# Kernel tuning notes

Measured on AMD Instinct MI355X. Metric: run time of the kernel, lower is better.

Reference implementation:

```python
import jax, jax.numpy as jnp
import numpy as np

D_MODEL = 1024
N_HEADS = 16
MAX_LEN = 2048
B, T = 2, 2048


def _rope_tables(seq_len, d_model):
    # NOTE: inv_freq spans full d_model (not d_head), matching the source module,
    # since RoPE is applied to q/k of shape (B, T, D) before the head split.
    inv_freq = 1.0 / 10000 ** (jnp.arange(0, d_model, 2, dtype=jnp.float32) / d_model)
    pos = jnp.arange(seq_len, dtype=jnp.float32)
    freqs = jnp.outer(pos, inv_freq)            # (T, D/2)
    return jnp.cos(freqs), jnp.sin(freqs)


def _apply_rope(x, cos, sin):
    # x: (B, T, D); cos/sin: (T, D/2)
    c = jnp.repeat(cos, 2, axis=-1)[None]       # (1, T, D)
    s = jnp.repeat(sin, 2, axis=-1)[None]
    xr = x.reshape(x.shape[0], x.shape[1], -1, 2)
    x_rot = jnp.stack([-xr[..., 1], xr[..., 0]], axis=-1).reshape(x.shape)
    return x * c + x_rot * s


def setup_inputs() -> dict:
    key = jax.random.key(0)
    ks = jax.random.split(key, 5)
    scale = 1.0 / np.sqrt(D_MODEL)
    x = jax.random.normal(ks[0], (B, T, D_MODEL), dtype=jnp.float32)
    wq = jax.random.normal(ks[1], (D_MODEL, D_MODEL), dtype=jnp.float32) * scale
    wk = jax.random.normal(ks[2], (D_MODEL, D_MODEL), dtype=jnp.float32) * scale
    wv = jax.random.normal(ks[3], (D_MODEL, D_MODEL), dtype=jnp.float32) * scale
    wo = jax.random.normal(ks[4], (D_MODEL, D_MODEL), dtype=jnp.float32) * scale
    mask = jnp.tril(jnp.ones((T, T), dtype=bool))[None, None]  # (1,1,T,T) causal
    return {"x": x, "mask": mask, "wq": wq, "wk": wk, "wv": wv, "wo": wo}


def reference(x, mask, wq, wk, wv, wo):
    Bn, Tn, Dn = x.shape
    d_head = Dn // N_HEADS
    cos, sin = _rope_tables(Tn, Dn)
    q = _apply_rope(x @ wq, cos, sin)
    k = _apply_rope(x @ wk, cos, sin)
    v = x @ wv
    q = q.reshape(Bn, Tn, N_HEADS, d_head).transpose(0, 2, 1, 3)  # (B,H,T,dh)
    k = k.reshape(Bn, Tn, N_HEADS, d_head).transpose(0, 2, 1, 3)
    v = v.reshape(Bn, Tn, N_HEADS, d_head).transpose(0, 2, 1, 3)
    scores = jnp.einsum('bhqd,bhkd->bhqk', q, k) / jnp.sqrt(jnp.float32(d_head))
    scores = jnp.where(mask, scores, jnp.float32(-1e10))
    attn = jax.nn.softmax(scores, axis=-1)
    out = jnp.einsum('bhqk,bhkd->bhqd', attn, v)
    out = out.transpose(0, 2, 1, 3).reshape(Bn, Tn, Dn)
    return out @ wo
```

## Files before the change

kernel.cpp:

```cpp
#include <hip/hip_runtime.h>
#include <hip/hip_bf16.h>

#define D_MODEL 1024
#define N_HEADS 16
#define DH      64
#define BATCH   2
#define SEQ     2048
#define M_ROWS  (BATCH*SEQ)

using f32x4  = __attribute__((ext_vector_type(4)))  float;
using f32x16 = __attribute__((ext_vector_type(16))) float;
using bfx8   = __attribute__((ext_vector_type(8)))  short;

__device__ __forceinline__ float bf2f(unsigned short u){
    unsigned int v = ((unsigned int)u) << 16;
    float f; __builtin_memcpy(&f, &v, 4); return f;
}
__device__ __forceinline__ unsigned short f2bf(float f){
    unsigned int u; __builtin_memcpy(&u, &f, 4);
    u = (u + 0x7FFFu + ((u >> 16) & 1u)) >> 16;
    return (unsigned short)u;
}
__device__ __forceinline__ unsigned int cvtpk_bf16(float lo, float hi){
    unsigned int r;
    asm("v_cvt_pk_bf16_f32 %0, %1, %2" : "=v"(r) : "v"(lo), "v"(hi));
    return r;
}

typedef __attribute__((address_space(3))) void as3_void;
typedef __attribute__((address_space(1))) const void as1_cvoid;
__device__ __forceinline__ void gload16(const void* g, void* l){
    __builtin_amdgcn_global_load_lds((as1_cvoid*)g, (as3_void*)l, 16, 0, 0);
}

__global__ void cast_x_kernel(const float* __restrict__ x, unsigned short* __restrict__ xb){
    int i = blockIdx.x*blockDim.x + threadIdx.x;
    float4 v = reinterpret_cast<const float4*>(x)[i];
    ushort4 o; o.x=f2bf(v.x); o.y=f2bf(v.y); o.z=f2bf(v.z); o.w=f2bf(v.w);
    reinterpret_cast<ushort4*>(xb)[i] = o;
}

__global__ void transpose_cast_w(const float* __restrict__ w0, const float* __restrict__ w1,
                                 const float* __restrict__ w2, const float* __restrict__ w3,
                                 unsigned short* __restrict__ o0, unsigned short* __restrict__ o1,
                                 unsigned short* __restrict__ o2, unsigned short* __restrict__ o3){
    __shared__ float tile[32][33];
    const float* w; unsigned short* o;
    switch (blockIdx.z){
        case 0:  w=w0; o=o0; break;
        case 1:  w=w1; o=o1; break;
        case 2:  w=w2; o=o2; break;
        default: w=w3; o=o3; break;
    }
    const int tx = threadIdx.x, ty = threadIdx.y;
    const int x0 = blockIdx.x*32, y0 = blockIdx.y*32;
    #pragma unroll
    for (int j=0;j<32;j+=8) tile[ty+j][tx] = w[(size_t)(y0+ty+j)*D_MODEL + x0 + tx];
    __syncthreads();
    #pragma unroll
    for (int j=0;j<32;j+=8) o[(size_t)(x0+ty+j)*D_MODEL + y0 + tx] = f2bf(tile[tx][ty+j]);
}

__global__ __launch_bounds__(256) void gemm_qkv(const unsigned short* __restrict__ A,
                                                const unsigned short* __restrict__ Bq,
                                                const unsigned short* __restrict__ Bk,
                                                const unsigned short* __restrict__ Bv,
                                                unsigned short* __restrict__ Qo,
                                                unsigned short* __restrict__ Ko,
                                                unsigned short* __restrict__ Vto){
    __shared__ unsigned short As[64*64];
    __shared__ unsigned short Bs[128*64];
    const int bid  = blockIdx.x;
    const int xcdg = bid & 7;
    const int i    = bid >> 3;
    const int yt   = xcdg*8 + (i & 7);
    const int xsel = i >> 3;
    const int sel  = xsel >> 3;
    const int n0   = (xsel & 7) * 128;
    const unsigned short* Bt = (sel==0) ? Bq : ((sel==1) ? Bk : Bv);
    const int tid = threadIdx.x;
    const int lane = tid & 63, wid = tid >> 6;
    const int l15 = lane & 15, hi = lane >> 4;
    const int wr = wid >> 1, wc = wid & 1;
    const int m0 = yt * 64;

    f32x4 acc[2][4] = {};

    for (int kt = 0; kt < D_MODEL; kt += 64){
        __syncthreads();
        #pragma unroll
        for (int i2 = 0; i2 < 2; ++i2){
            int c = tid + 256*i2;
            int row = c >> 3, ch = c & 7;
            int sc = ch ^ (row & 7);
            gload16(A + (size_t)(m0 + row)*D_MODEL + kt + sc*8, As + c*8);
        }
        #pragma unroll
        for (int i2 = 0; i2 < 4; ++i2){
            int c = tid + 256*i2;
            int row = c >> 3, ch = c & 7;
            int sc = ch ^ (row & 7);
            gload16(Bt + (size_t)(n0 + row)*D_MODEL + kt + sc*8, Bs + c*8);
        }
        asm volatile("s_waitcnt vmcnt(0)" ::: "memory");
        __syncthreads();
        #pragma unroll
        for (int ks = 0; ks < 2; ++ks){
            bfx8 a[2], b[4];
            #pragma unroll
            for (int t = 0; t < 2; ++t){
                const int ra = 32*wr + 16*t + l15;
                a[t] = *reinterpret_cast<const bfx8*>(As + ra*64 + (((ks*4 + hi) ^ (ra & 7))*8));
            }
            #pragma unroll
            for (int t = 0; t < 4; ++t){
                const int rb = 64*wc + 16*t + l15;
                b[t] = *reinterpret_cast<const bfx8*>(Bs + rb*64 + (((ks*4 + hi) ^ (rb & 7))*8));
            }
            #pragma unroll
            for (int rt = 0; rt < 2; ++rt)
                #pragma unroll
                for (int ct = 0; ct < 4; ++ct)
                    acc[rt][ct] = __builtin_amdgcn_mfma_f32_16x16x32_bf16(a[rt], b[ct], acc[rt][ct], 0, 0, 0);
        }
    }

    if (sel < 2){
        unsigned short* o = sel ? Ko : Qo;
        const float cfac = -0.02595256269f;
        float invf[4];
        #pragma unroll
        for (int ct = 0; ct < 4; ++ct){
            const int n = n0 + 64*wc + 16*ct + l15;
            invf[ct] = exp2f(cfac * (float)(n >> 1));
        }
        #pragma unroll
        for (int rt = 0; rt < 2; ++rt)
            #pragma unroll
            for (int ct = 0; ct < 4; ++ct){
                const int m = m0 + 32*wr + 16*rt + 4*hi;
                const int n = n0 + 64*wc + 16*ct + l15;
                #pragma unroll
                for (int r=0;r<4;++r){
                    float v = acc[rt][ct][r];
                    float prt = __shfl_xor(v, 1);
                    int tpos = (m + r) & (SEQ-1);
                    float ang = (float)tpos * invf[ct];
                    float sv = __sinf(ang), cv = __cosf(ang);
                    float rot = (n & 1) ? __builtin_fmaf(v, cv,  prt*sv)
                                        : __builtin_fmaf(v, cv, -(prt*sv));
                    o[(size_t)(m+r)*D_MODEL + n] = f2bf(rot);
                }
            }
    } else {
        #pragma unroll
        for (int rt = 0; rt < 2; ++rt)
            #pragma unroll
            for (int ct = 0; ct < 4; ++ct){
                const int m = m0 + 32*wr + 16*rt + 4*hi;
                const int n = n0 + 64*wc + 16*ct + l15;
                const int b  = m >> 11, t = m & (SEQ-1);
                const int h  = n >> 6,  d = n & 63;
                ushort4 pk;
                pk.x = f2bf(acc[rt][ct][0]); pk.y = f2bf(acc[rt][ct][1]);
                pk.z = f2bf(acc[rt][ct][2]); pk.w = f2bf(acc[rt][ct][3]);
                *reinterpret_cast<ushort4*>(Vto + ((size_t)((b*N_HEADS + h)*DH + d))*SEQ + t) = pk;
            }
    }
}

__global__ __launch_bounds__(256) void gemm_out(const unsigned short* __restrict__ A,
                                                const unsigned short* __restrict__ Bt,
                                                float* __restrict__ dst){
    __shared__ unsigned short As[64*64];
    __shared__ unsigned short Bs[128*64];
    const int tid = threadIdx.x;
    const int lane = tid & 63, wid = tid >> 6;
    const int l15 = lane & 15, hi = lane >> 4;
    const int wr = wid >> 1, wc = wid & 1;
    const int m0 = blockIdx.y * 64, n0 = blockIdx.x * 128;

    f32x4 acc[2][4] = {};

    for (int kt = 0; kt < D_MODEL; kt += 64){
        __syncthreads();
        #pragma unroll
        for (int i = 0; i < 2; ++i){
            int c = tid + 256*i;
            int row = c >> 3, ch = c & 7;
            int sc = ch ^ (row & 7);
            gload16(A + (size_t)(m0 + row)*D_MODEL + kt + sc*8, As + c*8);
        }
        #pragma unroll
        for (int i = 0; i < 4; ++i){
            int c = tid + 256*i;
            int row = c >> 3, ch = c & 7;
            int sc = ch ^ (row & 7);
            gload16(Bt + (size_t)(n0 + row)*D_MODEL + kt + sc*8, Bs + c*8);
        }
        asm volatile("s_waitcnt vmcnt(0)" ::: "memory");
        __syncthreads();
        #pragma unroll
        for (int ks = 0; ks < 2; ++ks){
            bfx8 a[2], b[4];
            #pragma unroll
            for (int t = 0; t < 2; ++t){
                const int ra = 32*wr + 16*t + l15;
                a[t] = *reinterpret_cast<const bfx8*>(As + ra*64 + (((ks*4 + hi) ^ (ra & 7))*8));
            }
            #pragma unroll
            for (int t = 0; t < 4; ++t){
                const int rb = 64*wc + 16*t + l15;
                b[t] = *reinterpret_cast<const bfx8*>(Bs + rb*64 + (((ks*4 + hi) ^ (rb & 7))*8));
            }
            #pragma unroll
            for (int rt = 0; rt < 2; ++rt)
                #pragma unroll
                for (int ct = 0; ct < 4; ++ct)
                    acc[rt][ct] = __builtin_amdgcn_mfma_f32_16x16x32_bf16(a[rt], b[ct], acc[rt][ct], 0, 0, 0);
        }
    }

    #pragma unroll
    for (int rt = 0; rt < 2; ++rt)
        #pragma unroll
        for (int ct = 0; ct < 4; ++ct){
            const int m = m0 + 32*wr + 16*rt + 4*hi;
            const int n = n0 + 64*wc + 16*ct + l15;
            #pragma unroll
            for (int r=0;r<4;++r) dst[(size_t)(m+r)*D_MODEL + n] = acc[rt][ct][r];
        }
}

__global__ __launch_bounds__(256, 2) void attn_kernel(const unsigned short* __restrict__ Q,
                                                      const unsigned short* __restrict__ K,
                                                      const unsigned short* __restrict__ Vt,
                                                      unsigned short* __restrict__ O){
    __shared__ float Olds[3][64][64];
    __shared__ float Llds[3][64];

    const int tid = threadIdx.x;
    const int lane = tid & 63, wid = tid >> 6;
    const int l31 = lane & 31, hi2 = (lane >> 5) & 1;
    const int bid = blockIdx.x;
    const int xcd = bid & 7, j = bid >> 3;
    const int hp  = xcd*4 + (j & 3);
    const int b = hp >> 4, h = hp & 15;
    const int qt2 = 31 - (j >> 2);
    const int skmax = 2*qt2 + 1;
    const int qrowA = qt2*64 + l31;
    const int qrowB = qrowA + 32;

    const unsigned short* Kbase = K  + (size_t)(b*SEQ)*D_MODEL + h*DH + 8*hi2;
    const unsigned short* Vbase = Vt + ((size_t)((b*N_HEADS + h)*DH))*SEQ + 8*hi2;
    const float k2 = 0.18033688011f;

    bfx8 qfA[4], qfB[4];
    {
        const unsigned short* qa = Q + ((size_t)(b*SEQ) + qrowA)*D_MODEL + h*DH + 8*hi2;
        const unsigned short* qb = Q + ((size_t)(b*SEQ) + qrowB)*D_MODEL + h*DH + 8*hi2;
        #pragma unroll
        for (int m=0;m<4;++m){
            qfA[m] = *reinterpret_cast<const bfx8*>(qa + 16*m);
            qfB[m] = *reinterpret_cast<const bfx8*>(qb + 16*m);
        }
    }

    f32x16 oaccA[2] = {}, oaccB[2] = {};
    float lA = 0.f, lB = 0.f;

    bfx8 kf[4];
    if (wid <= skmax){
        const unsigned short* kp = Kbase + (size_t)(wid*32 + l31)*D_MODEL;
        #pragma unroll
        for (int m=0;m<4;++m) kf[m] = *reinterpret_cast<const bfx8*>(kp + 16*m);
    }

    for (int sk = wid; sk <= skmax; sk += 4){
        bfx8 vf[2][2];
        #pragma unroll
        for (int dt=0; dt<2; ++dt)
            #pragma unroll
            for (int ks=0; ks<2; ++ks)
                vf[dt][ks] = *reinterpret_cast<const bfx8*>(Vbase + (size_t)(32*dt + l31)*SEQ + sk*32 + 16*ks);

        const bool doA = (sk < skmax);

        f32x16 stA = {}, stB = {};
        __builtin_amdgcn_s_setprio(1);
        #pragma unroll
        for (int m=0; m<4; ++m){
            if (doA) stA = __builtin_amdgcn_mfma_f32_32x32x16_bf16(kf[m], qfA[m], stA, 0,0,0);
            stB = __builtin_amdgcn_mfma_f32_32x32x16_bf16(kf[m], qfB[m], stB, 0,0,0);
        }
        __builtin_amdgcn_s_setprio(0);

        bfx8 kn[4];
        if (sk + 4 <= skmax){
            const unsigned short* kp = Kbase + (size_t)((sk+4)*32 + l31)*D_MODEL;
            #pragma unroll
            for (int m=0;m<4;++m) kn[m] = *reinterpret_cast<const bfx8*>(kp + 16*m);
        }

        float pA[16], pB[16];
        float rsA = 0.f, rsB = 0.f;
        const bool maskA = (sk == 2*qt2);
        const bool maskB = (sk == skmax);
        #pragma unroll
        for (int r=0;r<16;++r){
            int kg = sk*32 + (r&3) + 8*(r>>2) + 4*hi2;
            if (doA){
                float eA = (maskA && kg > qrowA) ? 0.f : exp2f(stA[r]*k2);
                pA[r] = eA; rsA += eA;
            }
            float eB = (maskB && kg > qrowB) ? 0.f : exp2f(stB[r]*k2);
            pB[r] = eB; rsB += eB;
        }
        if (doA){ rsA += __shfl_xor(rsA, 32); lA += rsA; }
        rsB += __shfl_xor(rsB, 32); lB += rsB;

        bfx8 paA0, paA1, paB0, paB1;
        if (doA){
            unsigned int c[8], x[8];
            #pragma unroll
            for (int q=0;q<8;++q) c[q] = cvtpk_bf16(pA[2*q], pA[2*q+1]);
            #pragma unroll
            for (int q=0;q<8;++q) x[q] = __shfl_xor(c[q], 32);
            uint4 w0 = (hi2==0) ? make_uint4(c[0],c[1],x[0],x[1]) : make_uint4(x[2],x[3],c[2],c[3]);
            uint4 w1 = (hi2==0) ? make_uint4(c[4],c[5],x[4],x[5]) : make_uint4(x[6],x[7],c[6],c[7]);
            paA0 = *reinterpret_cast<bfx8*>(&w0);
            paA1 = *reinterpret_cast<bfx8*>(&w1);
        }
        {
            unsigned int c[8], x[8];
            #pragma unroll
            for (int q=0;q<8;++q) c[q] = cvtpk_bf16(pB[2*q], pB[2*q+1]);
            #pragma unroll
            for (int q=0;q<8;++q) x[q] = __shfl_xor(c[q], 32);
            uint4 w0 = (hi2==0) ? make_uint4(c[0],c[1],x[0],x[1]) : make_uint4(x[2],x[3],c[2],c[3]);
            uint4 w1 = (hi2==0) ? make_uint4(c[4],c[5],x[4],x[5]) : make_uint4(x[6],x[7],c[6],c[7]);
            paB0 = *reinterpret_cast<bfx8*>(&w0);
            paB1 = *reinterpret_cast<bfx8*>(&w1);
        }

        __builtin_amdgcn_s_setprio(1);
        #pragma unroll
        for (int dt=0; dt<2; ++dt){
            if (doA){
                f32x16 o = oaccA[dt];
                o = __builtin_amdgcn_mfma_f32_32x32x16_bf16(paA0, vf[dt][0], o, 0,0,0);
                o = __builtin_amdgcn_mfma_f32_32x32x16_bf16(paA1, vf[dt][1], o, 0,0,0);
                oaccA[dt] = o;
            }
            f32x16 o = oaccB[dt];
            o = __builtin_amdgcn_mfma_f32_32x32x16_bf16(paB0, vf[dt][0], o, 0,0,0);
            o = __builtin_amdgcn_mfma_f32_32x32x16_bf16(paB1, vf[dt][1], o, 0,0,0);
            oaccB[dt] = o;
        }
        __builtin_amdgcn_s_setprio(0);

        #pragma unroll
        for (int m=0;m<4;++m) kf[m] = kn[m];
    }

    if (wid != 0){
        #pragma unroll
        for (int r=0; r<16; ++r){
            const int crow = (r&3) + 8*(r>>2) + 4*hi2;
            #pragma unroll
            for (int dt=0; dt<2; ++dt){
                Olds[wid-1][crow     ][32*dt + l31] = oaccA[dt][r];
                Olds[wid-1][crow + 32][32*dt + l31] = oaccB[dt][r];
            }
        }
        if (hi2 == 0){ Llds[wid-1][l31] = lA; Llds[wid-1][l31 + 32] = lB; }
    }
    __syncthreads();
    if (wid == 0){
        float la = lA, lb = lB;
        #pragma unroll
        for (int jj=0;jj<3;++jj){ la += Llds[jj][l31]; lb += Llds[jj][l31 + 32]; }
        float invA = 1.0f / la, invB = 1.0f / lb;
        #pragma unroll
        for (int r=0; r<16; ++r){
            const int crow = (r&3) + 8*(r>>2) + 4*hi2;
            float icA = __shfl(invA, crow);
            float icB = __shfl(invB, crow);
            #pragma unroll
            for (int dt=0; dt<2; ++dt){
                float va = oaccA[dt][r], vb = oaccB[dt][r];
                #pragma unroll
                for (int jj=0;jj<3;++jj){
                    va += Olds[jj][crow     ][32*dt + l31];
                    vb += Olds[jj][crow + 32][32*dt + l31];
                }
                const int rowA = qt2*64 + crow;
                O[((size_t)(b*SEQ) + rowA     )*D_MODEL + h*DH + 32*dt + l31] = f2bf(va * icA);
                O[((size_t)(b*SEQ) + rowA + 32)*D_MODEL + h*DH + 32*dt + l31] = f2bf(vb * icB);
            }
        }
    }
}

extern "C" void kernel_launch(void* const* d_in, const int* in_sizes, int n_in,
                              void* d_out, int out_size, void* d_ws, size_t ws_size,
                              hipStream_t stream) {
    const float* x  = (const float*)d_in[0];
    const float* wq = (const float*)d_in[2];
    const float* wk = (const float*)d_in[3];
    const float* wv = (const float*)d_in[4];
    const float* wo = (const float*)d_in[5];

    char* ws = (char*)d_ws;
    unsigned short* xb  = (unsigned short*)(ws);
    unsigned short* wqt = (unsigned short*)(ws + (8u  << 20));
    unsigned short* wkt = (unsigned short*)(ws + (10u << 20));
    unsigned short* wvt = (unsigned short*)(ws + (12u << 20));
    unsigned short* wot = (unsigned short*)(ws + (14u << 20));
    unsigned short* Qb  = (unsigned short*)(ws + (16u << 20));
    unsigned short* Kb  = (unsigned short*)(ws + (24u << 20));
    unsigned short* Vt  = (unsigned short*)(ws + (32u << 20));
    unsigned short* Ob  = (unsigned short*)(ws + (40u << 20));

    cast_x_kernel<<<M_ROWS*D_MODEL/4/256, 256, 0, stream>>>(x, xb);
    transpose_cast_w<<<dim3(32,32,4), dim3(32,8), 0, stream>>>(wq,wk,wv,wo, wqt,wkt,wvt,wot);

    gemm_qkv<<<1536, 256, 0, stream>>>(xb, wqt, wkt, wvt, Qb, Kb, Vt);

    attn_kernel<<<1024, 256, 0, stream>>>(Qb, Kb, Vt, Ob);

    gemm_out<<<dim3(8,64), 256, 0, stream>>>(Ob, wot, (float*)d_out);
}
```

Before: 114.9 us.

## Merge prep kernels and shrink output GEMM tiles with XCD-aware block mapping

The x cast and the weight transpose-cast are merged into one launch, with the block index split between the two jobs, which saves one kernel launch. The output projection GEMM moves from 64x128 tiles on a 2D grid to 64x64 tiles on a 1D grid of 1024 blocks. That grid uses an XCD-aware mapping so neighbouring M tiles share an XCD. The smaller tiles raise the block count to fill the CUs better, but each block reuses less data and global loads per FLOP go up.

Measured after the change: 112.0 us. -2.5%, faster.

```diff
diff --git a/kernel.cpp b/kernel.cpp
--- a/kernel.cpp
+++ b/kernel.cpp
@@ -33,27 +33,32 @@
     __builtin_amdgcn_global_load_lds((as1_cvoid*)g, (as3_void*)l, 16, 0, 0);
 }
 
-__global__ void cast_x_kernel(const float* __restrict__ x, unsigned short* __restrict__ xb){
-    int i = blockIdx.x*blockDim.x + threadIdx.x;
-    float4 v = reinterpret_cast<const float4*>(x)[i];
-    ushort4 o; o.x=f2bf(v.x); o.y=f2bf(v.y); o.z=f2bf(v.z); o.w=f2bf(v.w);
-    reinterpret_cast<ushort4*>(xb)[i] = o;
-}
-
-__global__ void transpose_cast_w(const float* __restrict__ w0, const float* __restrict__ w1,
-                                 const float* __restrict__ w2, const float* __restrict__ w3,
-                                 unsigned short* __restrict__ o0, unsigned short* __restrict__ o1,
-                                 unsigned short* __restrict__ o2, unsigned short* __restrict__ o3){
+__global__ __launch_bounds__(256) void prep_kernel(const float* __restrict__ x, unsigned short* __restrict__ xb,
+                                                   const float* __restrict__ w0, const float* __restrict__ w1,
+                                                   const float* __restrict__ w2, const float* __restrict__ w3,
+                                                   unsigned short* __restrict__ o0, unsigned short* __restrict__ o1,
+                                                   unsigned short* __restrict__ o2, unsigned short* __restrict__ o3){
+    const int bid = blockIdx.x;
+    if (bid < 4096){
+        int i = bid*256 + threadIdx.x;
+        float4 v = reinterpret_cast<const float4*>(x)[i];
+        ushort4 o; o.x=f2bf(v.x); o.y=f2bf(v.y); o.z=f2bf(v.z); o.w=f2bf(v.w);
+        reinterpret_cast<ushort4*>(xb)[i] = o;
+        return;
+    }
     __shared__ float tile[32][33];
+    const int t = bid - 4096;
+    const int selw = t >> 10;
+    const int xt = (t >> 5) & 31, ytt = t & 31;
     const float* w; unsigned short* o;
-    switch (blockIdx.z){
+    switch (selw){
         case 0:  w=w0; o=o0; break;
         case 1:  w=w1; o=o1; break;
         case 2:  w=w2; o=o2; break;
         default: w=w3; o=o3; break;
     }
-    const int tx = threadIdx.x, ty = threadIdx.y;
-    const int x0 = blockIdx.x*32, y0 = blockIdx.y*32;
+    const int tx = threadIdx.x & 31, ty = threadIdx.x >> 5;
+    const int x0 = xt*32, y0 = ytt*32;
     #pragma unroll
     for (int j=0;j<32;j+=8) tile[ty+j][tx] = w[(size_t)(y0+ty+j)*D_MODEL + x0 + tx];
     __syncthreads();
@@ -173,27 +178,32 @@
                                                 const unsigned short* __restrict__ Bt,
                                                 float* __restrict__ dst){
     __shared__ unsigned short As[64*64];
-    __shared__ unsigned short Bs[128*64];
+    __shared__ unsigned short Bs[64*64];
+    const int bid  = blockIdx.x;
+    const int xcdg = bid & 7;
+    const int i    = bid >> 3;
+    const int mt   = xcdg*8 + (i & 7);
+    const int nt   = i >> 3;
+    const int m0 = mt * 64, n0 = nt * 64;
     const int tid = threadIdx.x;
     const int lane = tid & 63, wid = tid >> 6;
     const int l15 = lane & 15, hi = lane >> 4;
     const int wr = wid >> 1, wc = wid & 1;
-    const int m0 = blockIdx.y * 64, n0 = blockIdx.x * 128;
-
-    f32x4 acc[2][4] = {};
+
+    f32x4 acc[2][2] = {};
 
     for (int kt = 0; kt < D_MODEL; kt += 64){
         __syncthreads();
         #pragma unroll
-        for (int i = 0; i < 2; ++i){
-            int c = tid + 256*i;
+        for (int i2 = 0; i2 < 2; ++i2){
+            int c = tid + 256*i2;
             int row = c >> 3, ch = c & 7;
             int sc = ch ^ (row & 7);
             gload16(A + (size_t)(m0 + row)*D_MODEL + kt + sc*8, As + c*8);
         }
         #pragma unroll
-        for (int i = 0; i < 4; ++i){
-            int c = tid + 256*i;
+        for (int i2 = 0; i2 < 2; ++i2){
+            int c = tid + 256*i2;
             int row = c >> 3, ch = c & 7;
             int sc = ch ^ (row & 7);
             gload16(Bt + (size_t)(n0 + row)*D_MODEL + kt + sc*8, Bs + c*8);
@@ -202,21 +212,18 @@
         __syncthreads();
         #pragma unroll
         for (int ks = 0; ks < 2; ++ks){
-            bfx8 a[2], b[4];
+            bfx8 a[2], b[2];
             #pragma unroll
             for (int t = 0; t < 2; ++t){
                 const int ra = 32*wr + 16*t + l15;
                 a[t] = *reinterpret_cast<const bfx8*>(As + ra*64 + (((ks*4 + hi) ^ (ra & 7))*8));
-            }
-            #pragma unroll
-            for (int t = 0; t < 4; ++t){
-                const int rb = 64*wc + 16*t + l15;
+                const int rb = 32*wc + 16*t + l15;
                 b[t] = *reinterpret_cast<const bfx8*>(Bs + rb*64 + (((ks*4 + hi) ^ (rb & 7))*8));
             }
             #pragma unroll
             for (int rt = 0; rt < 2; ++rt)
                 #pragma unroll
-                for (int ct = 0; ct < 4; ++ct)
+                for (int ct = 0; ct < 2; ++ct)
                     acc[rt][ct] = __builtin_amdgcn_mfma_f32_16x16x32_bf16(a[rt], b[ct], acc[rt][ct], 0, 0, 0);
         }
     }
@@ -224,9 +231,9 @@
     #pragma unroll
     for (int rt = 0; rt < 2; ++rt)
         #pragma unroll
-        for (int ct = 0; ct < 4; ++ct){
+        for (int ct = 0; ct < 2; ++ct){
             const int m = m0 + 32*wr + 16*rt + 4*hi;
-            const int n = n0 + 64*wc + 16*ct + l15;
+            const int n = n0 + 32*wc + 16*ct + l15;
             #pragma unroll
             for (int r=0;r<4;++r) dst[(size_t)(m+r)*D_MODEL + n] = acc[rt][ct][r];
         }
@@ -422,12 +429,11 @@
     unsigned short* Vt  = (unsigned short*)(ws + (32u << 20));
     unsigned short* Ob  = (unsigned short*)(ws + (40u << 20));
 
-    cast_x_kernel<<<M_ROWS*D_MODEL/4/256, 256, 0, stream>>>(x, xb);
-    transpose_cast_w<<<dim3(32,32,4), dim3(32,8), 0, stream>>>(wq,wk,wv,wo, wqt,wkt,wvt,wot);
+    prep_kernel<<<8192, 256, 0, stream>>>(x, xb, wq, wk, wv, wo, wqt, wkt, wvt, wot);
 
     gemm_qkv<<<1536, 256, 0, stream>>>(xb, wqt, wkt, wvt, Qb, Kb, Vt);
 
     attn_kernel<<<1024, 256, 0, stream>>>(Qb, Kb, Vt, Ob);
 
-    gemm_out<<<dim3(8,64), 256, 0, stream>>>(Ob, wot, (float*)d_out);
-}
+    gemm_out<<<1024, 256, 0, stream>>>(Ob, wot, (float*)d_out);
+}
```
